# Kernel optimization log

Hardware: AMD Instinct MI355X
Metric: run time of the kernel (lower is better)

## Reference

```python
import jax, jax.numpy as jnp
import numpy as np

N_CELLS = 20   # 10 opp + 10 gen LSTM cells
IN = 8
HID = 10


def setup_inputs() -> dict:
    key = jax.random.key(0)
    ks = jax.random.split(key, 13)
    s_ih = 1.0 / np.sqrt(HID)
    inp = {
        "x": jax.random.normal(ks[0], (1, 1, IN), jnp.float32),
        "h0": jax.random.normal(ks[1], (N_CELLS, HID), jnp.float32),
        "c0": jax.random.normal(ks[2], (N_CELLS, HID), jnp.float32),
        # Stacked per-cell LSTM params (PyTorch gate order: i, f, g, o)
        "W_ih": jax.random.uniform(ks[3], (N_CELLS, 4 * HID, IN), jnp.float32, -s_ih, s_ih),
        "W_hh": jax.random.uniform(ks[4], (N_CELLS, 4 * HID, HID), jnp.float32, -s_ih, s_ih),
        "b_ih": jax.random.uniform(ks[5], (N_CELLS, 4 * HID), jnp.float32, -s_ih, s_ih),
        "b_hh": jax.random.uniform(ks[6], (N_CELLS, 4 * HID), jnp.float32, -s_ih, s_ih),
        # Decoder MLP
        "W1": jax.random.uniform(ks[7], (50, 200), jnp.float32, -1 / np.sqrt(200), 1 / np.sqrt(200)),
        "b1": jax.random.uniform(ks[8], (50,), jnp.float32, -1 / np.sqrt(200), 1 / np.sqrt(200)),
        "W2": jax.random.uniform(ks[9], (10, 50), jnp.float32, -1 / np.sqrt(50), 1 / np.sqrt(50)),
        "b2": jax.random.uniform(ks[10], (10,), jnp.float32, -1 / np.sqrt(50), 1 / np.sqrt(50)),
        "W3": jax.random.uniform(ks[11], (1, 10), jnp.float32, -1 / np.sqrt(10), 1 / np.sqrt(10)),
        "b3": jax.random.uniform(ks[12], (1,), jnp.float32, -1 / np.sqrt(10), 1 / np.sqrt(10)),
    }
    return inp


def reference(x, h0, c0, W_ih, W_hh, b_ih, b_hh, W1, b1, W2, b2, W3, b3):
    # Single LSTM time step (seq=1, batch=1), batched across all 20 cells.
    xv = x.reshape(IN)
    gates = (jnp.einsum("kgi,i->kg", W_ih, xv)
             + jnp.einsum("kgh,kh->kg", W_hh, h0)
             + b_ih + b_hh)                        # [20, 40]
    i_g, f_g, g_g, o_g = jnp.split(gates, 4, axis=1)
    i_g = jax.nn.sigmoid(i_g)
    f_g = jax.nn.sigmoid(f_g)
    g_g = jnp.tanh(g_g)
    o_g = jax.nn.sigmoid(o_g)
    c = f_g * c0 + i_g * g_g                       # [20, 10]
    h = o_g * jnp.tanh(c)                          # [20, 10]
    # cells 0..9 are the opp bank, 10..19 the gen bank; decoder sees (gen, opp)
    feat = jnp.concatenate([h[10:].reshape(-1), h[:10].reshape(-1)])  # [200]
    h1 = jnp.tanh(W1 @ feat + b1)
    h2 = jnp.tanh(W2 @ h1 + b2)
    out = jnp.tanh(W3 @ h2 + b3)
    return out.reshape(1, 1, 1)
```

## Files before the change

kernel.cpp:

```cpp
#include <hip/hip_runtime.h>
#include <math.h>

#define NCELLS 20
#define INDIM  8
#define HID    10

__device__ __forceinline__ float sigmoidf_(float v) {
    return 1.0f / (1.0f + __expf(-v));
}

__global__ __launch_bounds__(256) void net_fused(
    const float* __restrict__ x,
    const float* __restrict__ h0,
    const float* __restrict__ c0,
    const float* __restrict__ W_ih,
    const float* __restrict__ W_hh,
    const float* __restrict__ b_ih,
    const float* __restrict__ b_hh,
    const float* __restrict__ W1,
    const float* __restrict__ b1,
    const float* __restrict__ W2,
    const float* __restrict__ b2,
    const float* __restrict__ W3,
    const float* __restrict__ b3,
    float* __restrict__ out)
{
    __shared__ float s_gates[NCELLS * 4 * HID];
    __shared__ float s_feat[200];
    __shared__ float s_h1[50];
    __shared__ float s_h2[10];

    const int tid = threadIdx.x;

    float xr[INDIM];
    #pragma unroll
    for (int i = 0; i < INDIM; ++i) xr[i] = x[i];

    for (int g = tid; g < NCELLS * 4 * HID; g += 256) {
        const int k = g / (4 * HID);
        const int r = g - k * (4 * HID);
        float acc = b_ih[g] + b_hh[g];
        const float* wi = W_ih + g * INDIM;
        #pragma unroll
        for (int i = 0; i < INDIM; ++i) acc = fmaf(wi[i], xr[i], acc);
        const float* wh = W_hh + g * HID;
        const float* hh = h0 + k * HID;
        #pragma unroll
        for (int j = 0; j < HID; ++j) acc = fmaf(wh[j], hh[j], acc);
        const int gt = r / HID;
        s_gates[g] = (gt == 2) ? tanhf(acc) : sigmoidf_(acc);
    }
    __syncthreads();

    if (tid < NCELLS * HID) {
        const int k = tid / HID, j = tid - k * HID;
        const float* gk = s_gates + k * (4 * HID);
        const float ig = gk[j];
        const float fg = gk[HID + j];
        const float gg = gk[2 * HID + j];
        const float og = gk[3 * HID + j];
        const float c  = fmaf(fg, c0[tid], ig * gg);
        const float h  = og * tanhf(c);
        const int pos = (k >= 10) ? (k - 10) * HID + j : 100 + k * HID + j;
        s_feat[pos] = h;
    }
    __syncthreads();

    if (tid < 200) {
        const int o = tid >> 2;
        const int p = tid & 3;
        float acc = 0.0f;
        const float* w = W1 + o * 200;
        for (int i = p; i < 200; i += 4) acc = fmaf(w[i], s_feat[i], acc);
        acc += __shfl_down(acc, 2, 4);
        acc += __shfl_down(acc, 1, 4);
        if (p == 0) s_h1[o] = tanhf(acc + b1[o]);
    }
    __syncthreads();

    if (tid < 10) {
        float acc = b2[tid];
        const float* w = W2 + tid * 50;
        #pragma unroll 10
        for (int i = 0; i < 50; ++i) acc = fmaf(w[i], s_h1[i], acc);
        s_h2[tid] = tanhf(acc);
    }
    __syncthreads();

    if (tid == 0) {
        float acc = b3[0];
        #pragma unroll
        for (int i = 0; i < 10; ++i) acc = fmaf(W3[i], s_h2[i], acc);
        out[0] = tanhf(acc);
    }
}

extern "C" void kernel_launch(void* const* d_in, const int* in_sizes, int n_in,
                              void* d_out, int out_size, void* d_ws, size_t ws_size,
                              hipStream_t stream) {
    const float* x    = (const float*)d_in[0];
    const float* h0   = (const float*)d_in[1];
    const float* c0   = (const float*)d_in[2];
    const float* W_ih = (const float*)d_in[3];
    const float* W_hh = (const float*)d_in[4];
    const float* b_ih = (const float*)d_in[5];
    const float* b_hh = (const float*)d_in[6];
    const float* W1   = (const float*)d_in[7];
    const float* b1   = (const float*)d_in[8];
    const float* W2   = (const float*)d_in[9];
    const float* b2   = (const float*)d_in[10];
    const float* W3   = (const float*)d_in[11];
    const float* b3   = (const float*)d_in[12];
    float* out = (float*)d_out;

    net_fused<<<1, 256, 0, stream>>>(x, h0, c0, W_ih, W_hh, b_ih, b_hh,
                                     W1, b1, W2, b2, W3, b3, out);
}
```

Baseline: 88.81 us.

## Split block into gate workers and decoder-weight prefetchers staged in shared memory

```diff
diff --git a/kernel.cpp b/kernel.cpp
--- a/kernel.cpp
+++ b/kernel.cpp
@@ -4,6 +4,8 @@
 #define NCELLS 20
 #define INDIM  8
 #define HID    10
+#define NGATES (NCELLS * 4 * HID)
+#define W1PAD  204
 
 __device__ __forceinline__ float sigmoidf_(float v) {
     return 1.0f / (1.0f + __expf(-v));
@@ -25,30 +27,85 @@
     const float* __restrict__ b3,
     float* __restrict__ out)
 {
-    __shared__ float s_gates[NCELLS * 4 * HID];
+    __shared__ float s_W1[50 * W1PAD];
+    __shared__ float s_W2[500];
+    __shared__ float s_gates[NGATES];
     __shared__ float s_feat[200];
     __shared__ float s_h1[50];
     __shared__ float s_h2[10];
+    __shared__ float s_b1[50];
+    __shared__ float s_b2[10];
+    __shared__ float s_w3[10];
+    __shared__ float s_b3[1];
 
     const int tid = threadIdx.x;
 
-    float xr[INDIM];
-    #pragma unroll
-    for (int i = 0; i < INDIM; ++i) xr[i] = x[i];
+    const float c0r = (tid < NCELLS * HID) ? c0[tid] : 0.0f;
 
-    for (int g = tid; g < NCELLS * 4 * HID; g += 256) {
-        const int k = g / (4 * HID);
-        const int r = g - k * (4 * HID);
-        float acc = b_ih[g] + b_hh[g];
-        const float* wi = W_ih + g * INDIM;
+    if (tid < 128) {
+        float xr[INDIM];
         #pragma unroll
-        for (int i = 0; i < INDIM; ++i) acc = fmaf(wi[i], xr[i], acc);
-        const float* wh = W_hh + g * HID;
-        const float* hh = h0 + k * HID;
+        for (int i = 0; i < INDIM; ++i) xr[i] = x[i];
+
+        for (int g = tid; g < NGATES; g += 128) {
+            const int k = g / (4 * HID);
+            const int r = g - k * (4 * HID);
+            float acc = b_ih[g] + b_hh[g];
+            const float4 wi0 = *(const float4*)(W_ih + g * INDIM);
+            const float4 wi1 = *(const float4*)(W_ih + g * INDIM + 4);
+            acc = fmaf(wi0.x, xr[0], acc);
+            acc = fmaf(wi0.y, xr[1], acc);
+            acc = fmaf(wi0.z, xr[2], acc);
+            acc = fmaf(wi0.w, xr[3], acc);
+            acc = fmaf(wi1.x, xr[4], acc);
+            acc = fmaf(wi1.y, xr[5], acc);
+            acc = fmaf(wi1.z, xr[6], acc);
+            acc = fmaf(wi1.w, xr[7], acc);
+            const float* wh = W_hh + g * HID;
+            const float* hh = h0 + k * HID;
+            #pragma unroll
+            for (int j = 0; j < HID; ++j) acc = fmaf(wh[j], hh[j], acc);
+            const int gt = r / HID;
+            s_gates[g] = (gt == 2) ? tanhf(acc) : sigmoidf_(acc);
+        }
+    } else {
+        const int l = tid - 128;
+        const float4* w1v = (const float4*)W1;
+
+        float4 w1buf[20];
         #pragma unroll
-        for (int j = 0; j < HID; ++j) acc = fmaf(wh[j], hh[j], acc);
-        const int gt = r / HID;
-        s_gates[g] = (gt == 2) ? tanhf(acc) : sigmoidf_(acc);
+        for (int j = 0; j < 19; ++j) w1buf[j] = w1v[l + 128 * j];
+        const bool extra = (l + 2432) < 2500;
+        if (extra) w1buf[19] = w1v[l + 2432];
+
+        const bool hasw2 = l < 125;
+        float4 w2buf;
+        if (hasw2) w2buf = ((const float4*)W2)[l];
+
+        float smallv = 0.0f;
+        if (l < 50)                smallv = b1[l];
+        else if (l < 60)           smallv = b2[l - 50];
+        else if (l < 70)           smallv = W3[l - 60];
+        else if (l == 70)          smallv = b3[0];
+
+        #pragma unroll
+        for (int j = 0; j < 19; ++j) {
+            const int m = l + 128 * j;
+            const int row = m / 50;
+            const int col = (m - row * 50) * 4;
+            *(float4*)&s_W1[row * W1PAD + col] = w1buf[j];
+        }
+        if (extra) {
+            const int m = l + 2432;
+            const int row = m / 50;
+            const int col = (m - row * 50) * 4;
+            *(float4*)&s_W1[row * W1PAD + col] = w1buf[19];
+        }
+        if (hasw2) *(float4*)&s_W2[l * 4] = w2buf;
+        if (l < 50)       s_b1[l] = smallv;
+        else if (l < 60)  s_b2[l - 50] = smallv;
+        else if (l < 70)  s_w3[l - 60] = smallv;
+        else if (l == 70) s_b3[0] = smallv;
     }
     __syncthreads();
 
@@ -59,7 +116,7 @@
         const float fg = gk[HID + j];
         const float gg = gk[2 * HID + j];
         const float og = gk[3 * HID + j];
-        const float c  = fmaf(fg, c0[tid], ig * gg);
+        const float c  = fmaf(fg, c0r, ig * gg);
         const float h  = og * tanhf(c);
         const int pos = (k >= 10) ? (k - 10) * HID + j : 100 + k * HID + j;
         s_feat[pos] = h;
@@ -69,28 +126,29 @@
     if (tid < 200) {
         const int o = tid >> 2;
         const int p = tid & 3;
+        const float* w = s_W1 + o * W1PAD;
         float acc = 0.0f;
-        const float* w = W1 + o * 200;
+        #pragma unroll
         for (int i = p; i < 200; i += 4) acc = fmaf(w[i], s_feat[i], acc);
         acc += __shfl_down(acc, 2, 4);
         acc += __shfl_down(acc, 1, 4);
-        if (p == 0) s_h1[o] = tanhf(acc + b1[o]);
+        if (p == 0) s_h1[o] = tanhf(acc + s_b1[o]);
     }
     __syncthreads();
 
     if (tid < 10) {
-        float acc = b2[tid];
-        const float* w = W2 + tid * 50;
-        #pragma unroll 10
+        float acc = s_b2[tid];
+        const float* w = s_W2 + tid * 50;
+        #pragma unroll
         for (int i = 0; i < 50; ++i) acc = fmaf(w[i], s_h1[i], acc);
         s_h2[tid] = tanhf(acc);
     }
     __syncthreads();
 
     if (tid == 0) {
-        float acc = b3[0];
+        float acc = s_b3[0];
         #pragma unroll
-        for (int i = 0; i < 10; ++i) acc = fmaf(W3[i], s_h2[i], acc);
+        for (int i = 0; i < 10; ++i) acc = fmaf(s_w3[i], s_h2[i], acc);
         out[0] = tanhf(acc);
     }
 }
```

Result: faster. 81.79 us (-7.9%).
